# Kernel tuning notes

Hardware: AMD Instinct MI355X
Metric: run time of the kernel (lower is better)

## Reference

```python
import jax, jax.numpy as jnp
import numpy as np

N_HEADS = 16
EMBED_DIM = 1024
HEAD_DIM = EMBED_DIM // N_HEADS
SRC_LEN = 128  # diagonal offset of the tril mask
B, T = 2, 2048


def setup_inputs() -> dict:
    key = jax.random.key(0)
    ks = jax.random.split(key, 7)
    s = 0.02
    return {
        "x": jax.random.normal(ks[0], (B, T, EMBED_DIM), dtype=jnp.float32),
        "Wq": jax.random.normal(ks[1], (EMBED_DIM, EMBED_DIM), dtype=jnp.float32) * s,
        "bq": jax.random.normal(ks[2], (EMBED_DIM,), dtype=jnp.float32) * s,
        "Wk": jax.random.normal(ks[3], (EMBED_DIM, EMBED_DIM), dtype=jnp.float32) * s,
        "bk": jax.random.normal(ks[4], (EMBED_DIM,), dtype=jnp.float32) * s,
        "Wv": jax.random.normal(ks[5], (EMBED_DIM, EMBED_DIM), dtype=jnp.float32) * s,
        "bv": jax.random.normal(ks[6], (EMBED_DIM,), dtype=jnp.float32) * s,
    }


def reference(x, Wq, bq, Wk, bk, Wv, bv):
    b, t, c = x.shape
    # project and split heads: [B, H, T, Dh]
    def heads(w, bias):
        y = x @ w.T + bias
        return y.reshape(b, t, N_HEADS, HEAD_DIM).transpose(0, 2, 1, 3)

    q = heads(Wq, bq)
    k = heads(Wk, bk)
    v = heads(Wv, bv)

    scale = HEAD_DIM ** -0.5
    attn = jnp.einsum("bhqd,bhkd->bhqk", q, k) * scale  # [B,H,T,T]
    # prefix-causal mask: key j allowed iff j <= i + SRC_LEN
    i = jnp.arange(t)[:, None]
    j = jnp.arange(t)[None, :]
    mask = j <= i + SRC_LEN  # [T, T]
    attn = jnp.where(mask[None, None], attn, -jnp.inf)
    attn = jax.nn.softmax(attn, axis=-1)
    # dropout p=0.0 -> identity in eval/reference
    out = jnp.einsum("bhqk,bhkd->bhqd", attn, v)  # [B,H,T,Dh]
    return out.transpose(0, 2, 1, 3).reshape(b, t, c)
```

## Files before the change

kernel.cpp:

```cpp
#include <hip/hip_runtime.h>
#include <hip/hip_bf16.h>

#define B_    2
#define T_    2048
#define C_    1024
#define H_    16
#define D_    64
#define SRCL_ 128

typedef short  short8 __attribute__((ext_vector_type(8)));
typedef float  f32x4  __attribute__((ext_vector_type(4)));
typedef unsigned short ushort4_t __attribute__((ext_vector_type(4)));

#define QSCALE 0.18033688011112042f

__device__ inline unsigned short f2bf(float f) {
    union { float f; unsigned u; } v; v.f = f;
    unsigned r = v.u + 0x7FFFu + ((v.u >> 16) & 1u);
    return (unsigned short)(r >> 16);
}

#if __has_builtin(__builtin_amdgcn_exp2f)
#define EXP2F(x) __builtin_amdgcn_exp2f(x)
#else
#define EXP2F(x) exp2f(x)
#endif

__device__ __forceinline__ void async_ld16(const void* g, void* l) {
    __builtin_amdgcn_global_load_lds(
        (const __attribute__((address_space(1))) unsigned int*)g,
        (__attribute__((address_space(3))) unsigned int*)l, 16, 0, 0);
}

__global__ __launch_bounds__(256) void convert_all(
        const float* __restrict__ x,
        const float* __restrict__ wq,
        const float* __restrict__ wk,
        const float* __restrict__ wv,
        unsigned short* __restrict__ xb,
        unsigned short* __restrict__ wb)
{
    const int NX = (B_ * T_ * C_) / 4;
    const int NW = (C_ * C_) / 4;
    int i = blockIdx.x * 256 + threadIdx.x;
    const float4* src;
    ushort4_t* dst;
    if (i < NX)               { src = (const float4*)x;  dst = (ushort4_t*)xb;                }
    else if (i < NX + NW)     { src = (const float4*)wq; dst = (ushort4_t*)wb;                i -= NX; }
    else if (i < NX + 2*NW)   { src = (const float4*)wk; dst = (ushort4_t*)(wb + C_*C_);      i -= NX + NW; }
    else                      { src = (const float4*)wv; dst = (ushort4_t*)(wb + 2*C_*C_);    i -= NX + 2*NW; }
    float4 v = src[i];
    ushort4_t o;
    o.x = f2bf(v.x); o.y = f2bf(v.y); o.z = f2bf(v.z); o.w = f2bf(v.w);
    dst[i] = o;
}

__global__ __launch_bounds__(256) void gemm_qkv(
        const unsigned short* __restrict__ xb,
        const unsigned short* __restrict__ wb,
        const float* __restrict__ bq,
        const float* __restrict__ bk,
        const float* __restrict__ bv,
        unsigned short* __restrict__ qo,
        unsigned short* __restrict__ kt,
        unsigned short* __restrict__ vt)
{
    __shared__ __align__(16) unsigned short As[128 * 32];
    __shared__ __align__(16) unsigned short Bs[128 * 32];
    __shared__ __align__(16) unsigned short Es[4][64 * 72];

    const int tid  = threadIdx.x;
    const int wave = tid >> 6;
    const int lane = tid & 63;
    const int lane15 = lane & 15;
    const int quad   = lane >> 4;
    const int wm = wave >> 1;
    const int wn = wave & 1;
    const int m0 = (blockIdx.x & 31) * 128;
    const int n0 = (blockIdx.x >> 5) * 128;

    f32x4 acc[4][4];
#pragma unroll
    for (int mi = 0; mi < 4; ++mi)
#pragma unroll
        for (int ni = 0; ni < 4; ++ni)
            acc[mi][ni] = (f32x4){0.f, 0.f, 0.f, 0.f};

    const int c0   = wave * 2;
    const int rowi0 = 16 * c0 + (lane >> 2);
    const int rowi1 = 16 * (c0 + 1) + (lane >> 2);
    const int col8 = (lane & 3) * 8;

    const unsigned short* xrow0 = &xb[(m0 + rowi0) * 1024 + col8];
    const unsigned short* xrow1 = &xb[(m0 + rowi1) * 1024 + col8];
    const unsigned short* wrow0 = &wb[(n0 + rowi0) * 1024 + col8];
    const unsigned short* wrow1 = &wb[(n0 + rowi1) * 1024 + col8];

    for (int k0 = 0; k0 < 1024; k0 += 32) {
        async_ld16(xrow0 + k0, &As[c0 * 512]);
        async_ld16(xrow1 + k0, &As[(c0 + 1) * 512]);
        async_ld16(wrow0 + k0, &Bs[c0 * 512]);
        async_ld16(wrow1 + k0, &Bs[(c0 + 1) * 512]);
        __syncthreads();

        short8 a[4], bf[4];
#pragma unroll
        for (int mi = 0; mi < 4; ++mi)
            a[mi] = *(const short8*)&As[(wm * 64 + mi * 16 + lane15) * 32 + quad * 8];
#pragma unroll
        for (int ni = 0; ni < 4; ++ni)
            bf[ni] = *(const short8*)&Bs[(wn * 64 + ni * 16 + lane15) * 32 + quad * 8];
#pragma unroll
        for (int mi = 0; mi < 4; ++mi)
#pragma unroll
            for (int ni = 0; ni < 4; ++ni)
                acc[mi][ni] = __builtin_amdgcn_mfma_f32_16x16x32_bf16(a[mi], bf[ni], acc[mi][ni], 0, 0, 0);
        __syncthreads();
    }

    const int colbase = n0 + wn * 64;
    const int which   = colbase >> 10;
    const int jj0     = colbase & 1023;
    const int h       = jj0 >> 6;
    const int rowbase = m0 + wm * 64;
    const int bidx    = rowbase >> 11;
    const int t0      = rowbase & 2047;
    const size_t bh   = (size_t)bidx * H_ + h;
    const float* bias_p = (which == 0 ? bq : (which == 1 ? bk : bv)) + jj0;

    unsigned short* stage = &Es[wave][0];

    if (which == 0) {
#pragma unroll
        for (int ni = 0; ni < 4; ++ni) {
            const float bias = bias_p[ni * 16 + lane15];
            const int d = ni * 16 + lane15;
#pragma unroll
            for (int mi = 0; mi < 4; ++mi)
#pragma unroll
                for (int r = 0; r < 4; ++r) {
                    const int tt = mi * 16 + quad * 4 + r;
                    stage[tt * 72 + d] = f2bf((acc[mi][ni][r] + bias) * QSCALE);
                }
        }
        unsigned short* gdst = qo + (bh * T_ + t0) * D_;
#pragma unroll
        for (int c = 0; c < 8; ++c) {
            const int idx = c * 64 + lane;
            const int row = idx >> 3;
            const int cc8 = (idx & 7) * 8;
            *(short8*)&gdst[idx * 8] = *(const short8*)&stage[row * 72 + cc8];
        }
    } else if (which == 1) {
#pragma unroll
        for (int ni = 0; ni < 4; ++ni) {
            const float bias = bias_p[ni * 16 + lane15];
            const int d = ni * 16 + lane15;
            const int dbase = (d >> 3) * 512 + (d & 7);
#pragma unroll
            for (int mi = 0; mi < 4; ++mi)
#pragma unroll
                for (int r = 0; r < 4; ++r) {
                    const int tt = mi * 16 + quad * 4 + r;
                    stage[dbase + tt * 8] = f2bf(acc[mi][ni][r] + bias);
                }
        }
        unsigned short* gdst = kt + bh * (size_t)(T_ * D_) + (t0 >> 6) * 4096;
#pragma unroll
        for (int c = 0; c < 8; ++c) {
            const int idx = c * 64 + lane;
            *(short8*)&gdst[idx * 8] = *(const short8*)&stage[idx * 8];
        }
    } else {
#pragma unroll
        for (int ni = 0; ni < 4; ++ni) {
            const float bias = bias_p[ni * 16 + lane15];
            const int d = ni * 16 + lane15;
#pragma unroll
            for (int mi = 0; mi < 4; ++mi)
#pragma unroll
                for (int r = 0; r < 4; ++r) {
                    const int tt = mi * 16 + quad * 4 + r;
                    stage[(tt >> 3) * 512 + d * 8 + (tt & 7)] = f2bf(acc[mi][ni][r] + bias);
                }
        }
        unsigned short* gdst = vt + bh * (size_t)(T_ * D_) + (t0 >> 6) * 4096;
#pragma unroll
        for (int c = 0; c < 8; ++c) {
            const int idx = c * 64 + lane;
            *(short8*)&gdst[idx * 8] = *(const short8*)&stage[idx * 8];
        }
    }
}

__global__ __launch_bounds__(256, 3) void attn(
        const unsigned short* __restrict__ qg,
        const unsigned short* __restrict__ kg,
        const unsigned short* __restrict__ vg,
        float* __restrict__ out)
{
    __shared__ __align__(16) unsigned short stage[2][8192];
    __shared__ __align__(16) unsigned short Ps[4][16 * 88];

    const int tid  = threadIdx.x;
    const int wave = tid >> 6;
    const int lane = tid & 63;
    const int lane15 = lane & 15;
    const int quad   = lane >> 4;

    const int bh = blockIdx.x & 31;
    const int a  = 31 - (blockIdx.x >> 5);
    const int b  = bh >> 4;
    const int h  = bh & 15;
    const int i0b = a * 64;
    const int i0  = i0b + wave * 16;

    const unsigned short* Q  = qg + (size_t)bh * T_ * D_;
    const unsigned short* KT = kg + (size_t)bh * T_ * D_;
    const unsigned short* VT = vg + (size_t)bh * T_ * D_;

    const short8 qf0 = *(const short8*)&Q[(i0 + lane15) * 64 + quad * 8];
    const short8 qf1 = *(const short8*)&Q[(i0 + lane15) * 64 + 32 + quad * 8];

    f32x4 o_acc[4];
#pragma unroll
    for (int di = 0; di < 4; ++di) o_acc[di] = (f32x4){0.f, 0.f, 0.f, 0.f};
    float l_p = 0.f;

    unsigned short* myPs = &Ps[wave][0];
    const int ntiles = min(a + 3, 32);
    const int limit  = i0 + lane15 + SRCL_;

    const int ib = wave * 4;
    const int loff = lane * 8;

#pragma unroll
    for (int c = 0; c < 4; ++c) {
        const int i = ib + c;
        const unsigned short* src = (i < 8) ? &KT[i * 512 + loff]
                                            : &VT[(i - 8) * 512 + loff];
        async_ld16(src, &stage[0][i * 512]);
    }

    for (int it = 0; it < ntiles; ++it) {
        const int jtn = min(it + 1, ntiles - 1);
        const unsigned short* sb = &stage[it & 1][0];
        unsigned short* nb = &stage[(it + 1) & 1][0];
#pragma unroll
        for (int c = 0; c < 4; ++c) {
            const int i = ib + c;
            const unsigned short* src = (i < 8) ? &KT[jtn * 4096 + i * 512 + loff]
                                                : &VT[jtn * 4096 + (i - 8) * 512 + loff];
            async_ld16(src, &nb[i * 512]);
        }
        __asm__ volatile("s_waitcnt vmcnt(4)\n\ts_barrier" ::: "memory");

        const int j0 = it << 6;
        f32x4 sv[4];
#pragma unroll
        for (int ni = 0; ni < 4; ++ni) {
            const short8 kf0 = *(const short8*)&sb[quad * 512 + (ni * 16 + lane15) * 8];
            const short8 kf1 = *(const short8*)&sb[(4 + quad) * 512 + (ni * 16 + lane15) * 8];
            f32x4 t = (f32x4){0.f, 0.f, 0.f, 0.f};
            t = __builtin_amdgcn_mfma_f32_16x16x32_bf16(kf0, qf0, t, 0, 0, 0);
            t = __builtin_amdgcn_mfma_f32_16x16x32_bf16(kf1, qf1, t, 0, 0, 0);
            sv[ni] = t;
        }

        if (j0 + 63 > i0 + SRCL_) {
#pragma unroll
            for (int ni = 0; ni < 4; ++ni)
#pragma unroll
                for (int r = 0; r < 4; ++r) {
                    const int key = j0 + ni * 16 + quad * 4 + r;
                    if (key > limit) sv[ni][r] = -INFINITY;
                }
        }

        float lacc = 0.f;
#pragma unroll
        for (int ni = 0; ni < 4; ++ni) {
            const float p0 = EXP2F(sv[ni][0]);
            const float p1 = EXP2F(sv[ni][1]);
            const float p2 = EXP2F(sv[ni][2]);
            const float p3 = EXP2F(sv[ni][3]);
            lacc += (p0 + p1) + (p2 + p3);
            const unsigned u0 = __float_as_uint(p0) + 0x8000u;
            const unsigned u1 = __float_as_uint(p1) + 0x8000u;
            const unsigned u2 = __float_as_uint(p2) + 0x8000u;
            const unsigned u3 = __float_as_uint(p3) + 0x8000u;
            uint2 w;
            w.x = __builtin_amdgcn_perm(u1, u0, 0x07060302);
            w.y = __builtin_amdgcn_perm(u3, u2, 0x07060302);
            *(uint2*)&myPs[lane15 * 88 + ni * 16 + quad * 4] = w;
        }
        l_p += lacc;

        const short8 pf0 = *(const short8*)&myPs[lane15 * 88 + quad * 8];
        const short8 pf1 = *(const short8*)&myPs[lane15 * 88 + 32 + quad * 8];

#pragma unroll
        for (int di = 0; di < 4; ++di) {
            const short8 vf0 = *(const short8*)&sb[4096 + quad * 512 + (di * 16 + lane15) * 8];
            const short8 vf1 = *(const short8*)&sb[4096 + (4 + quad) * 512 + (di * 16 + lane15) * 8];
            o_acc[di] = __builtin_amdgcn_mfma_f32_16x16x32_bf16(vf0, pf0, o_acc[di], 0, 0, 0);
            o_acc[di] = __builtin_amdgcn_mfma_f32_16x16x32_bf16(vf1, pf1, o_acc[di], 0, 0, 0);
        }

        __asm__ volatile("s_barrier" ::: "memory");
    }

    __asm__ volatile("s_waitcnt vmcnt(0)\n\ts_barrier" ::: "memory");

    float l0s = l_p + __shfl_xor(l_p, 16);
    const float inv = 1.0f / (l0s + __shfl_xor(l0s, 32));

    float* myOs = (float*)&stage[0][0] + wave * 2048;
#pragma unroll
    for (int di = 0; di < 4; ++di) {
        f32x4 v = o_acc[di] * inv;
        *(f32x4*)&myOs[lane15 * 68 + di * 16 + quad * 4] = v;
    }
    float* orow0 = out + ((size_t)(b * T_ + i0)) * C_ + h * 64;
#pragma unroll
    for (int c = 0; c < 4; ++c) {
        const int idx = c * 64 + lane;
        const int t   = idx >> 4;
        const int dc  = (idx & 15) * 4;
        float4 v = *(float4*)&myOs[t * 68 + dc];
        *(float4*)(orow0 + (size_t)t * C_ + dc) = v;
    }
}

extern "C" void kernel_launch(void* const* d_in, const int* in_sizes, int n_in,
                              void* d_out, int out_size, void* d_ws, size_t ws_size,
                              hipStream_t stream) {
    const float* x  = (const float*)d_in[0];
    const float* Wq = (const float*)d_in[1];
    const float* bq = (const float*)d_in[2];
    const float* Wk = (const float*)d_in[3];
    const float* bk = (const float*)d_in[4];
    const float* Wv = (const float*)d_in[5];
    const float* bv = (const float*)d_in[6];
    float* out = (float*)d_out;

    unsigned short* xb  = (unsigned short*)d_ws;
    unsigned short* wb  = xb  + (size_t)B_ * T_ * C_;
    unsigned short* qb  = wb  + (size_t)3 * C_ * C_;
    unsigned short* ktb = qb  + (size_t)B_ * H_ * T_ * D_;
    unsigned short* vtb = ktb + (size_t)B_ * H_ * T_ * D_;

    convert_all<<<7168, 256, 0, stream>>>(x, Wq, Wk, Wv, xb, wb);
    gemm_qkv<<<768, 256, 0, stream>>>(xb, wb, bq, bk, bv, qb, ktb, vtb);
    attn<<<1024, 256, 0, stream>>>(qb, ktb, vtb, out);
}
```

Baseline: 162.0 us.

## Double-buffer QKV GEMM loads and unify Q layout with K/V tiles

The QKV projection GEMM now double-buffers its A/B tiles in one shared buffer, prefetching the next k-slice while computing the current one, and shares that buffer with the epilogue staging to cut LDS use and allow 4 blocks per CU. Q is written in the same 8-wide chunked tile layout as K, with padded staging strides, and the attention kernel reads Q accordingly. The attention loop now waits for all loads, barriers, then issues the next prefetch, which removes the redundant last-tile load and one barrier per iteration. It also gives the prefetch less time to overlap with compute.

```diff
diff --git a/kernel.cpp b/kernel.cpp
--- a/kernel.cpp
+++ b/kernel.cpp
@@ -55,7 +55,7 @@
     dst[i] = o;
 }
 
-__global__ __launch_bounds__(256) void gemm_qkv(
+__global__ __launch_bounds__(256, 4) void gemm_qkv(
         const unsigned short* __restrict__ xb,
         const unsigned short* __restrict__ wb,
         const float* __restrict__ bq,
@@ -65,9 +65,7 @@
         unsigned short* __restrict__ kt,
         unsigned short* __restrict__ vt)
 {
-    __shared__ __align__(16) unsigned short As[128 * 32];
-    __shared__ __align__(16) unsigned short Bs[128 * 32];
-    __shared__ __align__(16) unsigned short Es[4][64 * 72];
+    __shared__ __align__(16) unsigned short uni[16640];
 
     const int tid  = threadIdx.x;
     const int wave = tid >> 6;
@@ -96,12 +94,25 @@
     const unsigned short* wrow0 = &wb[(n0 + rowi0) * 1024 + col8];
     const unsigned short* wrow1 = &wb[(n0 + rowi1) * 1024 + col8];
 
-    for (int k0 = 0; k0 < 1024; k0 += 32) {
-        async_ld16(xrow0 + k0, &As[c0 * 512]);
-        async_ld16(xrow1 + k0, &As[(c0 + 1) * 512]);
-        async_ld16(wrow0 + k0, &Bs[c0 * 512]);
-        async_ld16(wrow1 + k0, &Bs[(c0 + 1) * 512]);
-        __syncthreads();
+    async_ld16(xrow0, &uni[c0 * 512]);
+    async_ld16(xrow1, &uni[(c0 + 1) * 512]);
+    async_ld16(wrow0, &uni[4096 + c0 * 512]);
+    async_ld16(wrow1, &uni[4096 + (c0 + 1) * 512]);
+
+    for (int it = 0; it < 32; ++it) {
+        __asm__ volatile("s_waitcnt vmcnt(0)\n\ts_barrier" ::: "memory");
+
+        if (it + 1 < 32) {
+            const int k1 = (it + 1) * 32;
+            unsigned short* nb = &uni[((it + 1) & 1) * 8192];
+            async_ld16(xrow0 + k1, &nb[c0 * 512]);
+            async_ld16(xrow1 + k1, &nb[(c0 + 1) * 512]);
+            async_ld16(wrow0 + k1, &nb[4096 + c0 * 512]);
+            async_ld16(wrow1 + k1, &nb[4096 + (c0 + 1) * 512]);
+        }
+
+        const unsigned short* As = &uni[(it & 1) * 8192];
+        const unsigned short* Bs = As + 4096;
 
         short8 a[4], bf[4];
 #pragma unroll
@@ -115,8 +126,9 @@
 #pragma unroll
             for (int ni = 0; ni < 4; ++ni)
                 acc[mi][ni] = __builtin_amdgcn_mfma_f32_16x16x32_bf16(a[mi], bf[ni], acc[mi][ni], 0, 0, 0);
-        __syncthreads();
-    }
+    }
+
+    __syncthreads();
 
     const int colbase = n0 + wn * 64;
     const int which   = colbase >> 10;
@@ -127,69 +139,45 @@
     const int t0      = rowbase & 2047;
     const size_t bh   = (size_t)bidx * H_ + h;
     const float* bias_p = (which == 0 ? bq : (which == 1 ? bk : bv)) + jj0;
-
-    unsigned short* stage = &Es[wave][0];
-
-    if (which == 0) {
+    const float oscale  = (which == 0) ? QSCALE : 1.0f;
+
+    unsigned short* stage = &uni[wave * 4160];
+
+    if (which != 2) {
 #pragma unroll
         for (int ni = 0; ni < 4; ++ni) {
             const float bias = bias_p[ni * 16 + lane15];
             const int d = ni * 16 + lane15;
+            const int dbase = (d >> 3) * 520 + (d & 7);
 #pragma unroll
             for (int mi = 0; mi < 4; ++mi)
 #pragma unroll
                 for (int r = 0; r < 4; ++r) {
                     const int tt = mi * 16 + quad * 4 + r;
-                    stage[tt * 72 + d] = f2bf((acc[mi][ni][r] + bias) * QSCALE);
+                    stage[dbase + tt * 8] = f2bf((acc[mi][ni][r] + bias) * oscale);
                 }
         }
-        unsigned short* gdst = qo + (bh * T_ + t0) * D_;
-#pragma unroll
-        for (int c = 0; c < 8; ++c) {
-            const int idx = c * 64 + lane;
-            const int row = idx >> 3;
-            const int cc8 = (idx & 7) * 8;
-            *(short8*)&gdst[idx * 8] = *(const short8*)&stage[row * 72 + cc8];
-        }
-    } else if (which == 1) {
+    } else {
 #pragma unroll
         for (int ni = 0; ni < 4; ++ni) {
             const float bias = bias_p[ni * 16 + lane15];
             const int d = ni * 16 + lane15;
-            const int dbase = (d >> 3) * 512 + (d & 7);
 #pragma unroll
             for (int mi = 0; mi < 4; ++mi)
 #pragma unroll
                 for (int r = 0; r < 4; ++r) {
                     const int tt = mi * 16 + quad * 4 + r;
-                    stage[dbase + tt * 8] = f2bf(acc[mi][ni][r] + bias);
+                    stage[(tt >> 3) * 520 + d * 8 + (tt & 7)] = f2bf(acc[mi][ni][r] + bias);
                 }
         }
-        unsigned short* gdst = kt + bh * (size_t)(T_ * D_) + (t0 >> 6) * 4096;
-#pragma unroll
-        for (int c = 0; c < 8; ++c) {
-            const int idx = c * 64 + lane;
-            *(short8*)&gdst[idx * 8] = *(const short8*)&stage[idx * 8];
-        }
-    } else {
-#pragma unroll
-        for (int ni = 0; ni < 4; ++ni) {
-            const float bias = bias_p[ni * 16 + lane15];
-            const int d = ni * 16 + lane15;
-#pragma unroll
-            for (int mi = 0; mi < 4; ++mi)
-#pragma unroll
-                for (int r = 0; r < 4; ++r) {
-                    const int tt = mi * 16 + quad * 4 + r;
-                    stage[(tt >> 3) * 512 + d * 8 + (tt & 7)] = f2bf(acc[mi][ni][r] + bias);
-                }
-        }
-        unsigned short* gdst = vt + bh * (size_t)(T_ * D_) + (t0 >> 6) * 4096;
-#pragma unroll
-        for (int c = 0; c < 8; ++c) {
-            const int idx = c * 64 + lane;
-            *(short8*)&gdst[idx * 8] = *(const short8*)&stage[idx * 8];
-        }
+    }
+
+    unsigned short* gdst =
+        (which == 0 ? qo : (which == 1 ? kt : vt)) + bh * (size_t)(T_ * D_) + (t0 >> 6) * 4096;
+
+#pragma unroll
+    for (int c = 0; c < 8; ++c) {
+        *(short8*)&gdst[(c * 64 + lane) * 8] = *(const short8*)&stage[c * 520 + lane * 8];
     }
 }
 
@@ -212,15 +200,15 @@
     const int a  = 31 - (blockIdx.x >> 5);
     const int b  = bh >> 4;
     const int h  = bh & 15;
-    const int i0b = a * 64;
-    const int i0  = i0b + wave * 16;
+    const int i0 = a * 64 + wave * 16;
 
     const unsigned short* Q  = qg + (size_t)bh * T_ * D_;
     const unsigned short* KT = kg + (size_t)bh * T_ * D_;
     const unsigned short* VT = vg + (size_t)bh * T_ * D_;
 
-    const short8 qf0 = *(const short8*)&Q[(i0 + lane15) * 64 + quad * 8];
-    const short8 qf1 = *(const short8*)&Q[(i0 + lane15) * 64 + 32 + quad * 8];
+    const int qrow = wave * 16 + lane15;
+    const short8 qf0 = *(const short8*)&Q[a * 4096 + quad * 512 + qrow * 8];
+    const short8 qf1 = *(const short8*)&Q[a * 4096 + (4 + quad) * 512 + qrow * 8];
 
     f32x4 o_acc[4];
 #pragma unroll
@@ -243,19 +231,23 @@
     }
 
     for (int it = 0; it < ntiles; ++it) {
-        const int jtn = min(it + 1, ntiles - 1);
+        __asm__ volatile("s_waitcnt vmcnt(0)\n\ts_barrier" ::: "memory");
+
+        if (it + 1 < ntiles) {
+            unsigned short* nb = &stage[(it + 1) & 1][0];
+            const size_t tb = (size_t)(it + 1) * 4096;
+#pragma unroll
+            for (int c = 0; c < 4; ++c) {
+                const int i = ib + c;
+                const unsigned short* src = (i < 8) ? &KT[tb + i * 512 + loff]
+                                                    : &VT[tb + (i - 8) * 512 + loff];
+                async_ld16(src, &nb[i * 512]);
+            }
+        }
+
         const unsigned short* sb = &stage[it & 1][0];
-        unsigned short* nb = &stage[(it + 1) & 1][0];
-#pragma unroll
-        for (int c = 0; c < 4; ++c) {
-            const int i = ib + c;
-            const unsigned short* src = (i < 8) ? &KT[jtn * 4096 + i * 512 + loff]
-                                                : &VT[jtn * 4096 + (i - 8) * 512 + loff];
-            async_ld16(src, &nb[i * 512]);
-        }
-        __asm__ volatile("s_waitcnt vmcnt(4)\n\ts_barrier" ::: "memory");
-
         const int j0 = it << 6;
+
         f32x4 sv[4];
 #pragma unroll
         for (int ni = 0; ni < 4; ++ni) {
@@ -306,11 +298,9 @@
             o_acc[di] = __builtin_amdgcn_mfma_f32_16x16x32_bf16(vf0, pf0, o_acc[di], 0, 0, 0);
             o_acc[di] = __builtin_amdgcn_mfma_f32_16x16x32_bf16(vf1, pf1, o_acc[di], 0, 0, 0);
         }
-
-        __asm__ volatile("s_barrier" ::: "memory");
-    }
-
-    __asm__ volatile("s_waitcnt vmcnt(0)\n\ts_barrier" ::: "memory");
+    }
+
+    __syncthreads();
 
     float l0s = l_p + __shfl_xor(l_p, 16);
     const float inv = 1.0f / (l0s + __shfl_xor(l0s, 32));
```

Result: faster. 148.8 us (-8.1%).
